# Optimization experiments

Measured on AMD Instinct MI355X. Metric: run time of the kernel, lower is better.

## Reference

```python
import jax, jax.numpy as jnp
import numpy as np

L, B, T, D, H = 8, 4, 1024, 1024, 16
DH = D // H
TPB, NB = 16, 64  # tokens_per_block, max_blocks; T == TPB*NB
EPS = 1e-5


def _block_causal_mask():
    idx = jnp.arange(T)
    causal = idx[:, None] >= idx[None, :]
    blk = idx // TPB
    block_diag = blk[:, None] == blk[None, :]
    return causal | block_diag  # [T, T] bool


def _ln(x, g, b):
    mu = jnp.mean(x, axis=-1, keepdims=True)
    var = jnp.mean(jnp.square(x - mu), axis=-1, keepdims=True)
    return (x - mu) * jax.lax.rsqrt(var + EPS) * g + b


def setup_inputs() -> dict:
    key = jax.random.key(0)
    ks = jax.random.split(key, 8)
    s = 0.02
    inp = {
        'sequences': jax.random.normal(ks[0], (B, T, D), jnp.float32),
        'Wq': jax.random.normal(ks[1], (L, D, D), jnp.float32) * s,
        'bq': jnp.zeros((L, D), jnp.float32),
        'Wk': jax.random.normal(ks[2], (L, D, D), jnp.float32) * s,
        'bk': jnp.zeros((L, D), jnp.float32),
        'Wv': jax.random.normal(ks[3], (L, D, D), jnp.float32) * s,
        'bv': jnp.zeros((L, D), jnp.float32),
        'Wp': jax.random.normal(ks[4], (L, D, D), jnp.float32) * s,
        'bp': jnp.zeros((L, D), jnp.float32),
        'ln1_g': jnp.ones((L, D), jnp.float32),
        'ln1_b': jnp.zeros((L, D), jnp.float32),
        'ln2_g': jnp.ones((L, D), jnp.float32),
        'ln2_b': jnp.zeros((L, D), jnp.float32),
        'W1': jax.random.normal(ks[5], (L, D, 4 * D), jnp.float32) * s,
        'b1': jnp.zeros((L, 4 * D), jnp.float32),
        'W2': jax.random.normal(ks[6], (L, 4 * D, D), jnp.float32) * s,
        'b2': jnp.zeros((L, D), jnp.float32),
        'lnf_g': jnp.ones((D,), jnp.float32),
        'lnf_b': jnp.zeros((D,), jnp.float32),
    }
    return inp


def reference(sequences, Wq, bq, Wk, bk, Wv, bv, Wp, bp,
              ln1_g, ln1_b, ln2_g, ln2_b, W1, b1, W2, b2, lnf_g, lnf_b):
    mask = _block_causal_mask()
    scale = 1.0 / np.sqrt(DH)
    x = sequences
    for i in range(L):
        h = _ln(x, ln1_g[i], ln1_b[i])
        q = (h @ Wq[i] + bq[i]).reshape(B, T, H, DH)
        k = (h @ Wk[i] + bk[i]).reshape(B, T, H, DH)
        v = (h @ Wv[i] + bv[i]).reshape(B, T, H, DH)
        att = jnp.einsum('bthd,bshd->bhts', q, k) * scale  # [B,H,T,T]
        att = jnp.where(mask, att, -jnp.inf)
        att = jax.nn.softmax(att, axis=-1)
        y = jnp.einsum('bhts,bshd->bthd', att, v).reshape(B, T, D)
        x = x + (y @ Wp[i] + bp[i])
        h2 = _ln(x, ln2_g[i], ln2_b[i])
        ff = jax.nn.gelu(h2 @ W1[i] + b1[i], approximate=False) @ W2[i] + b2[i]
        x = x + ff
    return _ln(x, lnf_g, lnf_b)
```

## Files before the change

### kernel.cpp

```cpp
#include <hip/hip_runtime.h>
#include <hip/hip_bf16.h>
#include <math.h>

#define B_ 4
#define T_ 1024
#define D_ 1024
#define H_ 16
#define DH_ 64
#define M_ 4096
#define QSTR_ 3072
#define EPS_ 1e-5f

typedef __attribute__((ext_vector_type(4))) float f32x4;
typedef __attribute__((ext_vector_type(8))) short s16x8;

#if __has_builtin(__builtin_amdgcn_exp2f)
#define EXP2F __builtin_amdgcn_exp2f
#else
#define EXP2F exp2f
#endif

__device__ __forceinline__ float gelu_f(float x) {
  return 0.5f * x * (1.0f + erff(x * 0.70710678118654752f));
}
__device__ __forceinline__ float b2f(unsigned short u) {
  union { unsigned int i; float f; } c; c.i = ((unsigned int)u) << 16; return c.f;
}
__device__ __forceinline__ unsigned short f2b(float f) {
  __hip_bfloat16 h = __float2bfloat16(f);
  return *reinterpret_cast<unsigned short*>(&h);
}
__device__ __forceinline__ void g2l16(void* l, const void* g) {
  __builtin_amdgcn_global_load_lds(
      (const __attribute__((address_space(1))) void*)g,
      (__attribute__((address_space(3))) void*)l, 16, 0, 0);
}

struct TrAll {
  const float *wq, *wk, *wv, *wp, *w1, *w2;
  __hip_bfloat16 *dqkv, *dp, *d1, *d2;
};

template<bool BF16OUT, bool ADDP>
__device__ __forceinline__ void ln_body(
    int row, float* __restrict__ xio, const float* __restrict__ part,
    void* __restrict__ out,
    const float* __restrict__ g, const float* __restrict__ b) {
  const int tid = threadIdx.x;
  float* rp = xio + (size_t)row * D_;
  float4 v = *reinterpret_cast<const float4*>(rp + tid * 4);
  if (ADDP) {
    float4 pv = *reinterpret_cast<const float4*>(part + (size_t)row * D_ + tid * 4);
    v.x += pv.x; v.y += pv.y; v.z += pv.z; v.w += pv.w;
    *reinterpret_cast<float4*>(rp + tid * 4) = v;
  }
  float s = v.x + v.y + v.z + v.w;
  float s2 = v.x * v.x + v.y * v.y + v.z * v.z + v.w * v.w;
#pragma unroll
  for (int off = 1; off < 64; off <<= 1) {
    s += __shfl_xor(s, off);
    s2 += __shfl_xor(s2, off);
  }
  __shared__ float red[2][4];
  const int wid = tid >> 6;
  if ((tid & 63) == 0) { red[0][wid] = s; red[1][wid] = s2; }
  __syncthreads();
  s = red[0][0] + red[0][1] + red[0][2] + red[0][3];
  s2 = red[1][0] + red[1][1] + red[1][2] + red[1][3];
  const float mu = s * (1.0f / D_);
  const float var = s2 * (1.0f / D_) - mu * mu;
  const float rs = rsqrtf(var + EPS_);
  float4 gv = *reinterpret_cast<const float4*>(g + tid * 4);
  float4 bv = *reinterpret_cast<const float4*>(b + tid * 4);
  float o0 = (v.x - mu) * rs * gv.x + bv.x;
  float o1 = (v.y - mu) * rs * gv.y + bv.y;
  float o2 = (v.z - mu) * rs * gv.z + bv.z;
  float o3 = (v.w - mu) * rs * gv.w + bv.w;
  if (BF16OUT) {
    ushort4 pk;
    pk.x = f2b(o0); pk.y = f2b(o1); pk.z = f2b(o2); pk.w = f2b(o3);
    *reinterpret_cast<ushort4*>((unsigned short*)out + (size_t)row * D_ + tid * 4) = pk;
  } else {
    *reinterpret_cast<float4*>((float*)out + (size_t)row * D_ + tid * 4) =
        make_float4(o0, o1, o2, o3);
  }
}

template<bool BF16OUT, bool ADDP>
__global__ __launch_bounds__(256) void ln_kernel(
    float* __restrict__ xio, const float* __restrict__ part,
    void* __restrict__ out,
    const float* __restrict__ g, const float* __restrict__ b) {
  ln_body<BF16OUT, ADDP>(blockIdx.x, xio, part, out, g, b);
}

__device__ __forceinline__ void transpose_tile(
    const float* __restrict__ src, int sld,
    __hip_bfloat16* __restrict__ dst, int dld, int k0, int n0) {
  __shared__ float tile[32][33];
  const int t = threadIdx.x;
  const int r = t >> 3;
  const int cq = (t & 7) * 4;
  float4 vv = *reinterpret_cast<const float4*>(src + (size_t)(k0 + r) * sld + n0 + cq);
  tile[r][cq + 0] = vv.x; tile[r][cq + 1] = vv.y;
  tile[r][cq + 2] = vv.z; tile[r][cq + 3] = vv.w;
  __syncthreads();
  ushort4 o;
  o.x = f2b(tile[cq + 0][r]); o.y = f2b(tile[cq + 1][r]);
  o.z = f2b(tile[cq + 2][r]); o.w = f2b(tile[cq + 3][r]);
  *reinterpret_cast<ushort4*>((unsigned short*)dst + (size_t)(n0 + r) * dld + k0 + cq) = o;
}

__device__ __forceinline__ void transpose_dispatch(int t, const TrAll& a) {
  const float* src;
  __hip_bfloat16* dst;
  int sld, dld, k0, n0;
  if (t < 4096) {
    const int m = t >> 10, tile = t & 1023;
    k0 = (tile >> 5) * 32; n0 = (tile & 31) * 32;
    src = (m == 0) ? a.wq : (m == 1) ? a.wk : (m == 2) ? a.wv : a.wp;
    sld = 1024; dld = 1024;
    dst = (m < 3) ? (a.dqkv + (size_t)m * 1024 * 1024) : a.dp;
  } else if (t < 8192) {
    const int tile = t - 4096;
    k0 = (tile & 31) * 32; n0 = (tile >> 5) * 32;
    src = a.w1; sld = 4096; dst = a.d1; dld = 1024;
  } else {
    const int tile = t - 8192;
    k0 = (tile >> 5) * 32; n0 = (tile & 31) * 32;
    src = a.w2; sld = 1024; dst = a.d2; dld = 4096;
  }
  transpose_tile(src, sld, dst, dld, k0, n0);
}

template<bool ADDP>
__global__ __launch_bounds__(256) void ln_tr_fused(
    float* __restrict__ xio, const float* __restrict__ part,
    void* __restrict__ out,
    const float* __restrict__ g, const float* __restrict__ b, TrAll a) {
  if (blockIdx.x < M_) {
    ln_body<true, ADDP>(blockIdx.x, xio, part, out, g, b);
  } else {
    transpose_dispatch(blockIdx.x - M_, a);
  }
}

__global__ __launch_bounds__(256) void concat_bias(
    const float* __restrict__ bq, const float* __restrict__ bk,
    const float* __restrict__ bv, float* __restrict__ out) {
  const int i = blockIdx.x * 256 + threadIdx.x;
  const int l = i / QSTR_, c = i % QSTR_;
  const float* src = (c < 1024) ? bq : ((c < 2048) ? bk : bv);
  out[i] = src[l * 1024 + (c & 1023)];
}

template<int MODE, int BN>
__global__ __launch_bounds__(256) void gemm_mfma(
    const __hip_bfloat16* __restrict__ A,
    const __hip_bfloat16* __restrict__ Bt,
    const float* __restrict__ bias,
    void* __restrict__ Cout, int N, int K) {
  __shared__ short As[3][128 * 32];
  __shared__ short Bs[3][BN * 32];
  int bid = blockIdx.y * gridDim.x + blockIdx.x;
  const int nwg = gridDim.x * gridDim.y;
  bid = (bid & 7) * (nwg >> 3) + (bid >> 3);
  const int gn = (bid % gridDim.x) * BN;
  const int gm = (bid / gridDim.x) * 128;

  const int tid = threadIdx.x;
  const int wid = tid >> 6, lane = tid & 63;
  constexpr int MR = (BN == 128) ? 4 : 2;
  const int wm = (BN == 128) ? (wid >> 1) : wid;
  const int wn = (BN == 128) ? (wid & 1) : 0;
  const int fr = lane & 15, kg = lane >> 4;

  const int ldr = lane >> 2;
  const int ldk = (((lane & 3) ^ ((lane >> 3) & 3)) * 8);
  const unsigned short* ap =
      (const unsigned short*)A + (size_t)(gm + wid * 32 + ldr) * K + ldk;
  const unsigned short* bp =
      (const unsigned short*)Bt +
      (size_t)(gn + ((BN == 128) ? wid * 32 : wid * 16) + ldr) * K + ldk;

  const int nkt = K >> 5;

#define STAGE_T(t, buf)                                                    \
  {                                                                        \
    const unsigned short* a_ = ap + (size_t)(t) * 32;                      \
    g2l16((char*)As[buf] + (wid * 2) * 1024, a_);                          \
    g2l16((char*)As[buf] + (wid * 2 + 1) * 1024, a_ + (size_t)16 * K);     \
    const unsigned short* b_ = bp + (size_t)(t) * 32;                      \
    if (BN == 128) {                                                       \
      g2l16((char*)Bs[buf] + (wid * 2) * 1024, b_);                        \
      g2l16((char*)Bs[buf] + (wid * 2 + 1) * 1024, b_ + (size_t)16 * K);   \
    } else {                                                               \
      g2l16((char*)Bs[buf] + wid * 1024, b_);                              \
    }                                                                      \
  }

  STAGE_T(0, 0);
  STAGE_T(1, 1);

  const int cxa = (kg ^ ((fr >> 1) & 3)) * 8;
  f32x4 acc[MR][4] = {};
  for (int t = 0; t < nkt; ++t) {
    const int buf = t % 3;
    if (t + 2 < nkt) STAGE_T(t + 2, (t + 2) % 3);
    const int rem = nkt - 1 - t;
    if (rem >= 2) {
      if (BN == 128) asm volatile("s_waitcnt vmcnt(8)" ::: "memory");
      else           asm volatile("s_waitcnt vmcnt(6)" ::: "memory");
    } else if (rem == 1) {
      if (BN == 128) asm volatile("s_waitcnt vmcnt(4)" ::: "memory");
      else           asm volatile("s_waitcnt vmcnt(3)" ::: "memory");
    } else {
      asm volatile("s_waitcnt vmcnt(0)" ::: "memory");
    }
    __builtin_amdgcn_s_barrier();
    __builtin_amdgcn_sched_barrier(0);
    s16x8 af[MR], bfr[4];
#pragma unroll
    for (int m = 0; m < MR; ++m)
      af[m] = *reinterpret_cast<const s16x8*>(
          &As[buf][(wm * (16 * MR) + m * 16 + fr) * 32 + cxa]);
#pragma unroll
    for (int n = 0; n < 4; ++n)
      bfr[n] = *reinterpret_cast<const s16x8*>(
          &Bs[buf][(wn * 64 + n * 16 + fr) * 32 + cxa]);
#pragma unroll
    for (int m = 0; m < MR; ++m)
#pragma unroll
      for (int n = 0; n < 4; ++n)
        acc[m][n] = __builtin_amdgcn_mfma_f32_16x16x32_bf16(af[m], bfr[n], acc[m][n], 0, 0, 0);
    __builtin_amdgcn_sched_barrier(0);
    __builtin_amdgcn_s_barrier();
  }
#undef STAGE_T

  const int r0 = gm + wm * (16 * MR);
  const int c0 = gn + wn * 64;
  float bb[4];
#pragma unroll
  for (int n = 0; n < 4; ++n)
    bb[n] = bias ? bias[c0 + n * 16 + fr] : 0.0f;
#pragma unroll
  for (int m = 0; m < MR; ++m) {
#pragma unroll
    for (int j = 0; j < 4; ++j) {
      const int row = r0 + m * 16 + kg * 4 + j;
#pragma unroll
      for (int n = 0; n < 4; ++n) {
        float val = acc[m][n][j] + bb[n];
        const size_t idx = (size_t)row * N + c0 + n * 16 + fr;
        if (MODE == 0) {
          ((unsigned short*)Cout)[idx] = f2b(val);
        } else if (MODE == 1) {
          float* cp = (float*)Cout + idx;
          *cp = *cp + val;
        } else {
          ((unsigned short*)Cout)[idx] = f2b(gelu_f(val));
        }
      }
    }
  }
}

template<int MODE>
__global__ __launch_bounds__(512) void gemm_w256(
    const __hip_bfloat16* __restrict__ A,
    const __hip_bfloat16* __restrict__ Bt,
    const float* __restrict__ bias,
    void* __restrict__ Cout, float* __restrict__ P,
    int N, int K, int KS) {
  __shared__ short As[3][128 * 32];
  __shared__ short Bs[3][256 * 32];
  int bid = blockIdx.y * gridDim.x + blockIdx.x;
  const int nwg = gridDim.x * gridDim.y;
  bid = (bid & 7) * (nwg >> 3) + (bid >> 3);
  const int gn = (bid % gridDim.x) * 256;
  const int gm = (bid / gridDim.x) * 128;
  const int koff = (MODE == 3) ? blockIdx.z * KS : 0;

  const int tid = threadIdx.x;
  const int wid = tid >> 6, lane = tid & 63;
  const int wm = wid & 1, wn = wid >> 1;
  const int fr = lane & 15, kg = lane >> 4;

  const int ldr = lane >> 2;
  const int ldk = (((lane & 3) ^ ((lane >> 3) & 3)) * 8);
  const unsigned short* ap =
      (const unsigned short*)A + (size_t)(gm + wid * 16 + ldr) * K + koff + ldk;
  const unsigned short* bp =
      (const unsigned short*)Bt + (size_t)(gn + wid * 32 + ldr) * K + koff + ldk;

  const int nkt = ((MODE == 3) ? KS : K) >> 5;

#define STAGE_W(t, buf)                                                    \
  {                                                                        \
    g2l16((char*)As[buf] + wid * 1024, ap + (size_t)(t) * 32);             \
    const unsigned short* b_ = bp + (size_t)(t) * 32;                      \
    g2l16((char*)Bs[buf] + (wid * 2) * 1024, b_);                          \
    g2l16((char*)Bs[buf] + (wid * 2 + 1) * 1024, b_ + (size_t)16 * K);     \
  }

  STAGE_W(0, 0);
  STAGE_W(1, 1);

  const int cxa = (kg ^ ((fr >> 1) & 3)) * 8;
  f32x4 acc[4][4] = {};
  for (int t = 0; t < nkt; ++t) {
    const int buf = t % 3;
    if (t + 2 < nkt) STAGE_W(t + 2, (t + 2) % 3);
    const int rem = nkt - 1 - t;
    if (rem >= 2)      asm volatile("s_waitcnt vmcnt(6)" ::: "memory");
    else if (rem == 1) asm volatile("s_waitcnt vmcnt(3)" ::: "memory");
    else               asm volatile("s_waitcnt vmcnt(0)" ::: "memory");
    __builtin_amdgcn_s_barrier();
    __builtin_amdgcn_sched_barrier(0);
    s16x8 af[4], bfr[4];
#pragma unroll
    for (int m = 0; m < 4; ++m)
      af[m] = *reinterpret_cast<const s16x8*>(
          &As[buf][(wm * 64 + m * 16 + fr) * 32 + cxa]);
#pragma unroll
    for (int n = 0; n < 4; ++n)
      bfr[n] = *reinterpret_cast<const s16x8*>(
          &Bs[buf][(wn * 64 + n * 16 + fr) * 32 + cxa]);
#pragma unroll
    for (int m = 0; m < 4; ++m)
#pragma unroll
      for (int n = 0; n < 4; ++n)
        acc[m][n] = __builtin_amdgcn_mfma_f32_16x16x32_bf16(af[m], bfr[n], acc[m][n], 0, 0, 0);
    __builtin_amdgcn_sched_barrier(0);
    __builtin_amdgcn_s_barrier();
  }
#undef STAGE_W

  const int r0 = gm + wm * 64;
  const int c0 = gn + wn * 64;
  if (MODE == 3 && blockIdx.z == 1) {
#pragma unroll
    for (int m = 0; m < 4; ++m)
#pragma unroll
      for (int j = 0; j < 4; ++j) {
        const int row = r0 + m * 16 + kg * 4 + j;
#pragma unroll
        for (int n = 0; n < 4; ++n)
          P[(size_t)row * N + c0 + n * 16 + fr] = acc[m][n][j];
      }
    return;
  }
  float bb[4];
#pragma unroll
  for (int n = 0; n < 4; ++n)
    bb[n] = bias ? bias[c0 + n * 16 + fr] : 0.0f;
#pragma unroll
  for (int m = 0; m < 4; ++m) {
#pragma unroll
    for (int j = 0; j < 4; ++j) {
      const int row = r0 + m * 16 + kg * 4 + j;
#pragma unroll
      for (int n = 0; n < 4; ++n) {
        float val = acc[m][n][j] + bb[n];
        const size_t idx = (size_t)row * N + c0 + n * 16 + fr;
        if (MODE == 0) {
          ((unsigned short*)Cout)[idx] = f2b(val);
        } else if (MODE == 1 || MODE == 3) {
          float* cp = (float*)Cout + idx;
          *cp = *cp + val;
        } else {
          ((unsigned short*)Cout)[idx] = f2b(gelu_f(val));
        }
      }
    }
  }
}

__global__ __launch_bounds__(512) void gemm_8ph(
    const __hip_bfloat16* __restrict__ A,
    const __hip_bfloat16* __restrict__ Bt,
    const float* __restrict__ bias,
    unsigned short* __restrict__ Cout, int N, int K) {
  extern __shared__ short sm8[];
  int bid = blockIdx.y * gridDim.x + blockIdx.x;
  const int nwg = gridDim.x * gridDim.y;
  bid = (bid & 7) * (nwg >> 3) + (bid >> 3);
  const int gn = (bid % gridDim.x) * 256;
  const int gm = (bid / gridDim.x) * 256;
  const int tid = threadIdx.x;
  const int wid = tid >> 6, lane = tid & 63;
  const int wm = wid >> 2, wn = wid & 3;
  const int fr = lane & 15, kg = lane >> 4;
  const int r8 = lane >> 3, cp = lane & 7;
  const unsigned short* Ap = (const unsigned short*)A;
  const unsigned short* Bp = (const unsigned short*)Bt;
  const int nkt = K >> 6;

#define STAGE8(t, hbase, u)                                                  \
  {                                                                          \
    const int row_ = (u) * 64 + wid * 8 + r8;                                \
    const int c16_ = cp ^ (row_ & 7);                                        \
    g2l16((hbase) + ((u) * 64 + wid * 8) * 128,                              \
          Ap + (size_t)(gm + row_) * K + (size_t)(t) * 64 + c16_ * 8);       \
    g2l16((hbase) + 32768 + ((u) * 64 + wid * 8) * 128,                      \
          Bp + (size_t)(gn + row_) * K + (size_t)(t) * 64 + c16_ * 8);       \
  }

#pragma unroll
  for (int u = 0; u < 4; ++u) STAGE8(0, (char*)sm8, u);
  asm volatile("s_waitcnt vmcnt(0)" ::: "memory");
  __builtin_amdgcn_s_barrier();

  f32x4 acc[8][4] = {};
  for (int t = 0; t < nkt; ++t) {
    char* cur = (char*)sm8 + (t & 1) * 65536;
    char* nxt = (char*)sm8 + ((t & 1) ^ 1) * 65536;
    __builtin_amdgcn_sched_barrier(0);
#pragma unroll
    for (int p = 0; p < 4; ++p) {
      if (t + 1 < nkt) STAGE8(t + 1, nxt, p);
      s16x8 af[2][2], bfr[4][2];
#pragma unroll
      for (int mm = 0; mm < 2; ++mm) {
        const int row = wm * 128 + (p * 2 + mm) * 16 + fr;
#pragma unroll
        for (int kk = 0; kk < 2; ++kk)
          af[mm][kk] = *reinterpret_cast<const s16x8*>(
              cur + row * 128 + (((kk * 4 + kg) ^ (row & 7)) << 4));
      }
#pragma unroll
      for (int n = 0; n < 4; ++n) {
        const int row = wn * 64 + n * 16 + fr;
#pragma unroll
        for (int kk = 0; kk < 2; ++kk)
          bfr[n][kk] = *reinterpret_cast<const s16x8*>(
              cur + 32768 + row * 128 + (((kk * 4 + kg) ^ (row & 7)) << 4));
      }
      __builtin_amdgcn_s_setprio(1);
#pragma unroll
      for (int kk = 0; kk < 2; ++kk)
#pragma unroll
        for (int mm = 0; mm < 2; ++mm)
#pragma unroll
          for (int n = 0; n < 4; ++n)
            acc[p * 2 + mm][n] = __builtin_amdgcn_mfma_f32_16x16x32_bf16(
                af[mm][kk], bfr[n][kk], acc[p * 2 + mm][n], 0, 0, 0);
      __builtin_amdgcn_s_setprio(0);
    }
    if (t + 1 < nkt) {
      asm volatile("s_waitcnt vmcnt(0)" ::: "memory");
      __builtin_amdgcn_s_barrier();
    }
  }
#undef STAGE8

  const int r0 = gm + wm * 128;
  const int c0 = gn + wn * 64;
  float bb[4];
#pragma unroll
  for (int n = 0; n < 4; ++n) bb[n] = bias[c0 + n * 16 + fr];
#pragma unroll
  for (int m = 0; m < 8; ++m)
#pragma unroll
    for (int j = 0; j < 4; ++j) {
      const int row = r0 + m * 16 + kg * 4 + j;
#pragma unroll
      for (int n = 0; n < 4; ++n)
        Cout[(size_t)row * N + c0 + n * 16 + fr] =
            f2b(gelu_f(acc[m][n][j] + bb[n]));
    }
}

__global__ __launch_bounds__(512) void attn_mfma(
    const __hip_bfloat16* __restrict__ qkv, __hip_bfloat16* __restrict__ yg) {
  const int x = blockIdx.x;
  const int qb = (x < 2) ? (3 - x) : (x - 2);
  const int hh = blockIdx.y;
  const int bb = blockIdx.z;
  __shared__ short Qs[256 * 64];
  __shared__ short Ks[3][64 * 64];
  __shared__ short Vt[2][64 * 64];
  const int tid = threadIdx.x;
  const int wid = tid >> 6, lane = tid & 63;
  const int fr = lane & 15, kg = lane >> 4;
  const size_t qb_base = (size_t)bb * T_ * QSTR_ + (size_t)hh * DH_;
  const unsigned short* qgp = (const unsigned short*)qkv + qb_base;
  const unsigned short* kgp = qgp + 1024;
  const unsigned short* vgp = qgp + 2048;
  const float C = 0.125f * 1.4426950408889634f;

  const int r8 = lane >> 3, cp = lane & 7;
#pragma unroll
  for (int u = 0; u < 4; ++u) {
    const int row = wid * 32 + u * 8 + r8;
    const int c16 = cp ^ (row & 7);
    g2l16((char*)Qs + (wid * 32 + u * 8) * 128,
          qgp + (size_t)(qb * 256 + row) * QSTR_ + c16 * 8);
  }
  {
    const int row = wid * 8 + r8;
    const int c16 = cp ^ (row & 7);
    g2l16((char*)Ks[0] + (wid * 8) * 128, kgp + (size_t)row * QSTR_ + c16 * 8);
  }
  const int kv0 = tid >> 3;
  const int d0 = (tid & 7) * 8;
  const int rot = tid & 7;
  s16x8 sva = *reinterpret_cast<const s16x8*>(vgp + (size_t)kv0 * QSTR_ + d0);

  asm volatile("s_waitcnt vmcnt(0)" ::: "memory");
  __syncthreads();
  s16x8 qf[2][2];
#pragma unroll
  for (int rg = 0; rg < 2; ++rg) {
    const int row = wid * 32 + rg * 16 + fr;
    const char* rp = (const char*)Qs + row * 128;
    qf[rg][0] = *reinterpret_cast<const s16x8*>(rp + (((0 + kg) ^ (row & 7)) << 4));
    qf[rg][1] = *reinterpret_cast<const s16x8*>(rp + (((4 + kg) ^ (row & 7)) << 4));
  }

  f32x4 acco[2][4] = {};
  float m_run[2] = {-INFINITY, -INFINITY};
  float l_run[2] = {0.f, 0.f};

  const int q16hi = qb * 16 + wid * 2 + 1;
  const int ntile = 4 * qb + 4;
  for (int kt = 0; kt < ntile; ++kt) {
    const int kb3 = kt % 3;
    const int vb = kt & 1;
    asm volatile("s_waitcnt vmcnt(0)" ::: "memory");
#pragma unroll
    for (int j = 0; j < 8; ++j) {
      const int jj = (j + rot) & 7;
      const int d = d0 + jj;
      *(short*)((char*)Vt[vb] + d * 128 + ((((kv0 >> 3) ^ jj) & 7) << 4) + (kv0 & 7) * 2) = sva[jj];
    }
    if (kt + 1 < ntile) {
      const int row = wid * 8 + r8;
      const int c16 = cp ^ (row & 7);
      g2l16((char*)Ks[(kt + 1) % 3] + (wid * 8) * 128,
            kgp + (size_t)((kt + 1) * 64 + row) * QSTR_ + c16 * 8);
      sva = *reinterpret_cast<const s16x8*>(
          vgp + (size_t)((kt + 1) * 64 + kv0) * QSTR_ + d0);
    }
    __syncthreads();
    __builtin_amdgcn_sched_barrier(0);

    if (kt * 4 <= q16hi) {
      f32x4 accs[2][4] = {};
      __builtin_amdgcn_s_setprio(1);
#pragma unroll
      for (int n = 0; n < 4; ++n) {
        const int row = n * 16 + fr;
        const char* rp = (const char*)Ks[kb3] + row * 128;
        s16x8 kf0 = *reinterpret_cast<const s16x8*>(rp + (((0 + kg) ^ (row & 7)) << 4));
        s16x8 kf1 = *reinterpret_cast<const s16x8*>(rp + (((4 + kg) ^ (row & 7)) << 4));
#pragma unroll
        for (int rg = 0; rg < 2; ++rg) {
          accs[rg][n] = __builtin_amdgcn_mfma_f32_16x16x32_bf16(kf0, qf[rg][0], accs[rg][n], 0, 0, 0);
          accs[rg][n] = __builtin_amdgcn_mfma_f32_16x16x32_bf16(kf1, qf[rg][1], accs[rg][n], 0, 0, 0);
        }
      }
      __builtin_amdgcn_s_setprio(0);
#pragma unroll
      for (int rg = 0; rg < 2; ++rg) {
        const int q16 = qb * 16 + wid * 2 + rg;
        float mloc = -3.0e38f;
#pragma unroll
        for (int n = 0; n < 4; ++n)
          if (kt * 4 + n <= q16)
#pragma unroll
            for (int j = 0; j < 4; ++j) mloc = fmaxf(mloc, accs[rg][n][j]);
        mloc = fmaxf(mloc, __shfl_xor(mloc, 16));
        mloc = fmaxf(mloc, __shfl_xor(mloc, 32));
        if (!__all((mloc - m_run[rg]) * C <= 8.0f)) {
          const float mn = fmaxf(m_run[rg], mloc);
          const float a_ = EXP2F((m_run[rg] - mn) * C);
          m_run[rg] = mn;
          l_run[rg] *= a_;
          float aj[4];
#pragma unroll
          for (int j = 0; j < 4; ++j) aj[j] = __shfl(a_, kg * 4 + j);
#pragma unroll
          for (int dt = 0; dt < 4; ++dt)
#pragma unroll
            for (int j = 0; j < 4; ++j) acco[rg][dt][j] *= aj[j];
        }
        const float mn = m_run[rg];
        const int prow = wid * 32 + rg * 16 + fr;
        char* pbase = (char*)Qs + prow * 128 + (kg & 1) * 8;
        const int rxor = prow & 7;
        float psum = 0.f;
#pragma unroll
        for (int n = 0; n < 4; ++n) {
          const bool dead = (kt * 4 + n > q16);
          unsigned long long pk = 0;
#pragma unroll
          for (int j = 0; j < 4; ++j) {
            const float p = dead ? 0.0f : EXP2F((accs[rg][n][j] - mn) * C);
            psum += p;
            pk |= (unsigned long long)f2b(p) << (16 * j);
          }
          *reinterpret_cast<unsigned long long*>(
              pbase + (((n * 2 + (kg >> 1)) ^ rxor) << 4)) = pk;
        }
        l_run[rg] += psum;
      }
      __builtin_amdgcn_s_setprio(1);
#pragma unroll
      for (int rg = 0; rg < 2; ++rg) {
        const int prow = wid * 32 + rg * 16 + fr;
        const char* pp = (const char*)Qs + prow * 128;
#pragma unroll
        for (int kk = 0; kk < 2; ++kk) {
          const s16x8 pf = *reinterpret_cast<const s16x8*>(
              pp + ((((kk * 4 + kg) ^ (prow & 7)) & 7) << 4));
#pragma unroll
          for (int dt = 0; dt < 4; ++dt) {
            const int vrow = dt * 16 + fr;
            const s16x8 vf = *reinterpret_cast<const s16x8*>(
                (const char*)Vt[vb] + vrow * 128 + ((((kk * 4 + kg) ^ (vrow & 7)) & 7) << 4));
            acco[rg][dt] = __builtin_amdgcn_mfma_f32_16x16x32_bf16(pf, vf, acco[rg][dt], 0, 0, 0);
          }
        }
      }
      __builtin_amdgcn_s_setprio(0);
    }
  }

  unsigned short* yp = (unsigned short*)yg + (size_t)bb * T_ * D_ + (size_t)hh * DH_;
#pragma unroll
  for (int rg = 0; rg < 2; ++rg) {
    float lt = l_run[rg];
    lt += __shfl_xor(lt, 16);
    lt += __shfl_xor(lt, 32);
    const float linv = 1.0f / lt;
    float lj[4];
#pragma unroll
    for (int j = 0; j < 4; ++j) lj[j] = __shfl(linv, kg * 4 + j);
#pragma unroll
    for (int dt = 0; dt < 4; ++dt)
#pragma unroll
      for (int j = 0; j < 4; ++j) {
        const int row = qb * 256 + wid * 32 + rg * 16 + kg * 4 + j;
        yp[(size_t)row * D_ + dt * 16 + fr] = f2b(acco[rg][dt][j] * lj[j]);
      }
  }
}

extern "C" void kernel_launch(void* const* d_in, const int* in_sizes, int n_in,
                              void* d_out, int out_size, void* d_ws, size_t ws_size,
                              hipStream_t stream) {
  (void)in_sizes; (void)n_in; (void)out_size; (void)ws_size;
  const float* seq  = (const float*)d_in[0];
  const float* Wq   = (const float*)d_in[1];
  const float* bq   = (const float*)d_in[2];
  const float* Wk   = (const float*)d_in[3];
  const float* bk   = (const float*)d_in[4];
  const float* Wv   = (const float*)d_in[5];
  const float* bv   = (const float*)d_in[6];
  const float* Wp   = (const float*)d_in[7];
  const float* bp   = (const float*)d_in[8];
  const float* ln1g = (const float*)d_in[9];
  const float* ln1b = (const float*)d_in[10];
  const float* ln2g = (const float*)d_in[11];
  const float* ln2b = (const float*)d_in[12];
  const float* W1   = (const float*)d_in[13];
  const float* b1   = (const float*)d_in[14];
  const float* W2   = (const float*)d_in[15];
  const float* b2   = (const float*)d_in[16];
  const float* lnfg = (const float*)d_in[17];
  const float* lnfb = (const float*)d_in[18];

  float* x = (float*)d_out;
  char* ws = (char*)d_ws;
  const size_t MB = 1024ull * 1024ull;
  typedef __hip_bfloat16 bf16;
  bf16*  wtqkv = (bf16*)(ws + 0 * MB);
  bf16*  wtp   = (bf16*)(ws + 6 * MB);
  bf16*  wtF1  = (bf16*)(ws + 8 * MB);
  bf16*  wtF2  = (bf16*)(ws + 16 * MB);
  bf16*  hb    = (bf16*)(ws + 24 * MB);
  bf16*  qkv   = (bf16*)(ws + 32 * MB);
  bf16*  mid   = (bf16*)(ws + 56 * MB);
  float* bqkv  = (float*)(ws + 88 * MB);
  float* part  = (float*)(ws + 32 * MB);

  hipMemcpyAsync(x, seq, (size_t)M_ * D_ * sizeof(float), hipMemcpyDeviceToDevice, stream);

  const dim3 blk(256);
  const dim3 blkw(512);
  concat_bias<<<96, blk, 0, stream>>>(bq, bk, bv, bqkv);

  for (int i = 0; i < 8; ++i) {
    const size_t wo  = (size_t)i * D_ * D_;
    const size_t vo  = (size_t)i * D_;
    const size_t w1o = (size_t)i * D_ * 4 * D_;

    TrAll ta;
    ta.wq = Wq + wo; ta.wk = Wk + wo; ta.wv = Wv + wo; ta.wp = Wp + wo;
    ta.w1 = W1 + w1o; ta.w2 = W2 + w1o;
    ta.dqkv = wtqkv; ta.dp = wtp; ta.d1 = wtF1; ta.d2 = wtF2;
    if (i == 0)
      ln_tr_fused<false><<<16384, blk, 0, stream>>>(x, nullptr, hb, ln1g + vo, ln1b + vo, ta);
    else
      ln_tr_fused<true><<<16384, blk, 0, stream>>>(x, part, hb, ln1g + vo, ln1b + vo, ta);
    gemm_w256<0><<<dim3(12, 32), blkw, 0, stream>>>(
        hb, wtqkv, bqkv + (size_t)i * QSTR_, qkv, nullptr, QSTR_, 1024, 0);
    attn_mfma<<<dim3(4, 16, 4), blkw, 0, stream>>>(qkv, hb);
    gemm_mfma<1, 64><<<dim3(16, 32), blk, 0, stream>>>(hb, wtp, bp + vo, x, 1024, 1024);
    ln_kernel<true, false><<<M_, blk, 0, stream>>>(x, nullptr, hb, ln2g + vo, ln2b + vo);
    gemm_8ph<<<dim3(16, 16), blkw, 131072, stream>>>(
        hb, wtF1, b1 + (size_t)i * 4096, (unsigned short*)mid, 4096, 1024);
    gemm_w256<3><<<dim3(4, 32, 2), blkw, 0, stream>>>(
        mid, wtF2, b2 + vo, x, part, 1024, 4096, 2048);
  }
  ln_kernel<false, true><<<M_, blk, 0, stream>>>(x, part, x, lnfg, lnfb);
}
```

Baseline: 2.017 ms.

## Split attention KV range across blocks with flash-decoding style combine

Each (batch, head) now gets eight attention blocks instead of four. The KV range of the longer query blocks is split into chunks of at most six tiles, so work per block is balanced and the grid is twice as large. Partial unnormalized outputs plus running max and sum go to workspace in fp32, and a new combine kernel merges them into bf16 output. This costs an extra launch and fp32 partial traffic (about 29MB written and read back), and it reuses the mid buffer region as scratch.

Result: slower. 2.084 ms (+3.3%).

```diff
diff --git a/kernel.cpp b/kernel.cpp
--- a/kernel.cpp
+++ b/kernel.cpp
@@ -472,12 +472,21 @@
     }
 }
 
+__constant__ int QBT[8]  = {2, 2, 3, 3, 3, 0, 1, 1};
+__constant__ int KT0[8]  = {0, 6, 10, 0, 5, 0, 0, 4};
+__constant__ int KT1[8]  = {6, 12, 16, 5, 10, 4, 4, 8};
+__constant__ int SLOT[8] = {2, 3, 6, 4, 5, -1, 0, 1};
+
 __global__ __launch_bounds__(512) void attn_mfma(
-    const __hip_bfloat16* __restrict__ qkv, __hip_bfloat16* __restrict__ yg) {
-  const int x = blockIdx.x;
-  const int qb = (x < 2) ? (3 - x) : (x - 2);
+    const __hip_bfloat16* __restrict__ qkv, __hip_bfloat16* __restrict__ yg,
+    float* __restrict__ Opart, float* __restrict__ Ml) {
+  const int ch = blockIdx.x;
+  const int qb = QBT[ch];
+  const int kt0 = KT0[ch], kt1 = KT1[ch];
+  const int slot = SLOT[ch];
   const int hh = blockIdx.y;
   const int bb = blockIdx.z;
+  const int hbid = bb * 16 + hh;
   __shared__ short Qs[256 * 64];
   __shared__ short Ks[3][64 * 64];
   __shared__ short Vt[2][64 * 64];
@@ -501,12 +510,14 @@
   {
     const int row = wid * 8 + r8;
     const int c16 = cp ^ (row & 7);
-    g2l16((char*)Ks[0] + (wid * 8) * 128, kgp + (size_t)row * QSTR_ + c16 * 8);
+    g2l16((char*)Ks[0] + (wid * 8) * 128,
+          kgp + (size_t)(kt0 * 64 + row) * QSTR_ + c16 * 8);
   }
   const int kv0 = tid >> 3;
   const int d0 = (tid & 7) * 8;
   const int rot = tid & 7;
-  s16x8 sva = *reinterpret_cast<const s16x8*>(vgp + (size_t)kv0 * QSTR_ + d0);
+  s16x8 sva = *reinterpret_cast<const s16x8*>(
+      vgp + (size_t)(kt0 * 64 + kv0) * QSTR_ + d0);
 
   asm volatile("s_waitcnt vmcnt(0)" ::: "memory");
   __syncthreads();
@@ -524,10 +535,10 @@
   float l_run[2] = {0.f, 0.f};
 
   const int q16hi = qb * 16 + wid * 2 + 1;
-  const int ntile = 4 * qb + 4;
-  for (int kt = 0; kt < ntile; ++kt) {
-    const int kb3 = kt % 3;
-    const int vb = kt & 1;
+  for (int kt = kt0; kt < kt1; ++kt) {
+    const int rk = kt - kt0;
+    const int kb3 = rk % 3;
+    const int vb = rk & 1;
     asm volatile("s_waitcnt vmcnt(0)" ::: "memory");
 #pragma unroll
     for (int j = 0; j < 8; ++j) {
@@ -535,10 +546,10 @@
       const int d = d0 + jj;
       *(short*)((char*)Vt[vb] + d * 128 + ((((kv0 >> 3) ^ jj) & 7) << 4) + (kv0 & 7) * 2) = sva[jj];
     }
-    if (kt + 1 < ntile) {
+    if (kt + 1 < kt1) {
       const int row = wid * 8 + r8;
       const int c16 = cp ^ (row & 7);
-      g2l16((char*)Ks[(kt + 1) % 3] + (wid * 8) * 128,
+      g2l16((char*)Ks[(rk + 1) % 3] + (wid * 8) * 128,
             kgp + (size_t)((kt + 1) * 64 + row) * QSTR_ + c16 * 8);
       sva = *reinterpret_cast<const s16x8*>(
           vgp + (size_t)((kt + 1) * 64 + kv0) * QSTR_ + d0);
@@ -628,24 +639,77 @@
     }
   }
 
-  unsigned short* yp = (unsigned short*)yg + (size_t)bb * T_ * D_ + (size_t)hh * DH_;
-#pragma unroll
-  for (int rg = 0; rg < 2; ++rg) {
-    float lt = l_run[rg];
-    lt += __shfl_xor(lt, 16);
-    lt += __shfl_xor(lt, 32);
-    const float linv = 1.0f / lt;
-    float lj[4];
-#pragma unroll
-    for (int j = 0; j < 4; ++j) lj[j] = __shfl(linv, kg * 4 + j);
-#pragma unroll
-    for (int dt = 0; dt < 4; ++dt)
-#pragma unroll
-      for (int j = 0; j < 4; ++j) {
-        const int row = qb * 256 + wid * 32 + rg * 16 + kg * 4 + j;
-        yp[(size_t)row * D_ + dt * 16 + fr] = f2b(acco[rg][dt][j] * lj[j]);
-      }
-  }
+  if (slot < 0) {
+    unsigned short* yp = (unsigned short*)yg + (size_t)bb * T_ * D_ + (size_t)hh * DH_;
+#pragma unroll
+    for (int rg = 0; rg < 2; ++rg) {
+      float lt = l_run[rg];
+      lt += __shfl_xor(lt, 16);
+      lt += __shfl_xor(lt, 32);
+      const float linv = 1.0f / lt;
+      float lj[4];
+#pragma unroll
+      for (int j = 0; j < 4; ++j) lj[j] = __shfl(linv, kg * 4 + j);
+#pragma unroll
+      for (int dt = 0; dt < 4; ++dt)
+#pragma unroll
+        for (int j = 0; j < 4; ++j) {
+          const int row = qb * 256 + wid * 32 + rg * 16 + kg * 4 + j;
+          yp[(size_t)row * D_ + dt * 16 + fr] = f2b(acco[rg][dt][j] * lj[j]);
+        }
+    }
+  } else {
+    float* op = Opart + (size_t)(hbid * 7 + slot) * 256 * 64;
+    float* ml = Ml + (size_t)(hbid * 7 + slot) * 256 * 2;
+#pragma unroll
+    for (int rg = 0; rg < 2; ++rg) {
+      float lt = l_run[rg];
+      lt += __shfl_xor(lt, 16);
+      lt += __shfl_xor(lt, 32);
+      if (kg == 0) {
+        const int r = wid * 32 + rg * 16 + fr;
+        ml[r * 2] = m_run[rg];
+        ml[r * 2 + 1] = lt;
+      }
+#pragma unroll
+      for (int dt = 0; dt < 4; ++dt)
+#pragma unroll
+        for (int j = 0; j < 4; ++j) {
+          const int r = wid * 32 + rg * 16 + kg * 4 + j;
+          op[r * 64 + dt * 16 + fr] = acco[rg][dt][j];
+        }
+    }
+  }
+}
+
+__global__ __launch_bounds__(256) void attn_combine(
+    const float* __restrict__ Opart, const float* __restrict__ Ml,
+    __hip_bfloat16* __restrict__ yg) {
+  const int xq = blockIdx.x;
+  const int qbm = xq >> 6;
+  const int rg4 = xq & 63;
+  const int hh = blockIdx.y, bb = blockIdx.z;
+  const int hbid = bb * 16 + hh;
+  const int t = threadIdx.x;
+  const int r = rg4 * 4 + (t >> 6);
+  const int col = t & 63;
+  const int s0t[3] = {0, 2, 4};
+  const int cntt[3] = {2, 2, 3};
+  const int s0 = s0t[qbm], cnt = cntt[qbm];
+  const float C = 0.125f * 1.4426950408889634f;
+  float m = -INFINITY;
+  for (int c = 0; c < cnt; ++c)
+    m = fmaxf(m, Ml[((size_t)(hbid * 7 + s0 + c) * 256 + r) * 2]);
+  float lsum = 0.f, osum = 0.f;
+  for (int c = 0; c < cnt; ++c) {
+    const size_t mli = ((size_t)(hbid * 7 + s0 + c) * 256 + r) * 2;
+    const float w = EXP2F((Ml[mli] - m) * C);
+    lsum += Ml[mli + 1] * w;
+    osum += Opart[((size_t)(hbid * 7 + s0 + c) * 256 + r) * 64 + col] * w;
+  }
+  const int row = (qbm + 1) * 256 + r;
+  ((unsigned short*)yg)[(size_t)bb * T_ * D_ + (size_t)row * D_ + hh * DH_ + col] =
+      f2b(osum / lsum);
 }
 
 extern "C" void kernel_launch(void* const* d_in, const int* in_sizes, int n_in,
@@ -685,6 +749,8 @@
   bf16*  mid   = (bf16*)(ws + 56 * MB);
   float* bqkv  = (float*)(ws + 88 * MB);
   float* part  = (float*)(ws + 32 * MB);
+  float* aOp   = (float*)(ws + 56 * MB);
+  float* aMl   = (float*)(ws + 56 * MB + 29360128);
 
   hipMemcpyAsync(x, seq, (size_t)M_ * D_ * sizeof(float), hipMemcpyDeviceToDevice, stream);
 
@@ -707,7 +773,8 @@
       ln_tr_fused<true><<<16384, blk, 0, stream>>>(x, part, hb, ln1g + vo, ln1b + vo, ta);
     gemm_w256<0><<<dim3(12, 32), blkw, 0, stream>>>(
         hb, wtqkv, bqkv + (size_t)i * QSTR_, qkv, nullptr, QSTR_, 1024, 0);
-    attn_mfma<<<dim3(4, 16, 4), blkw, 0, stream>>>(qkv, hb);
+    attn_mfma<<<dim3(8, 16, 4), blkw, 0, stream>>>(qkv, hb, aOp, aMl);
+    attn_combine<<<dim3(192, 16, 4), blk, 0, stream>>>(aOp, aMl, hb);
     gemm_mfma<1, 64><<<dim3(16, 32), blk, 0, stream>>>(hb, wtp, bp + vo, x, 1024, 1024);
     ln_kernel<true, false><<<M_, blk, 0, stream>>>(x, nullptr, hb, ln2g + vo, ln2b + vo);
     gemm_8ph<<<dim3(16, 16), blkw, 131072, stream>>>(
```
